# Optimization experiments

Measured on AMD Instinct MI355X. Metric: run time of the kernel, lower is better.

## Reference

```python
import jax, jax.numpy as jnp
import numpy as np

N, NS, D, HID = 8192, 512, 1024, 1024  # nodes, num_edges, f_dim, mlp hidden (max(f_dim,128))


def layernorm(x, g, b, eps=1e-5):
    m = x.mean(-1, keepdims=True)
    v = x.var(-1, keepdims=True)
    return (x - m) / jnp.sqrt(v + eps) * g + b


def mask_topk(a, kk):
    # keep only the top-kk entries of each row (vectorized version of mask_attn)
    _, idx = jax.lax.top_k(a, kk)
    rows = jnp.arange(a.shape[0])[:, None]
    mask = jnp.zeros(a.shape, a.dtype).at[rows, idx].set(1.0)
    return a * mask


def setup_inputs() -> dict:
    key = jax.random.key(0)
    ks = jax.random.split(key, 16)
    xavier = lambda k, i, o: jax.random.uniform(k, (i, o), jnp.float32, -1.0, 1.0) * np.sqrt(6.0 / (i + o))
    return {
        "inputs": jax.random.normal(ks[0], (N, D), jnp.float32),
        "noise": jax.random.normal(ks[1], (NS, D), jnp.float32),
        "edges_mu": jax.random.normal(ks[2], (1, D), jnp.float32),
        "edges_logsigma": xavier(ks[3], 1, D),
        "Wq": xavier(ks[4], D, D), "bq": jnp.zeros((D,), jnp.float32),
        "Wk": xavier(ks[5], D, D), "bk": jnp.zeros((D,), jnp.float32),
        "Wv": xavier(ks[6], D, D), "bv": jnp.zeros((D,), jnp.float32),
        "W1": xavier(ks[7], 2 * D, HID), "b1": jnp.zeros((HID,), jnp.float32),
        "W2": xavier(ks[8], HID, D), "b2": jnp.zeros((D,), jnp.float32),
        "g_in": jnp.ones((D,), jnp.float32), "b_in": jnp.zeros((D,), jnp.float32),
        "g_e": jnp.ones((D,), jnp.float32), "b_e": jnp.zeros((D,), jnp.float32),
        "k_n": 64,
        "k_e": 8,
    }


def reference(inputs, noise, edges_mu, edges_logsigma, Wq, bq, Wk, bk, Wv, bv,
              W1, b1, W2, b2, g_in, b_in, g_e, b_e, k_n, k_e):
    n, d = inputs.shape
    scale = d ** -0.5
    eps = 1e-8
    x = layernorm(inputs, g_in, b_in)                       # norm_input
    k = jax.nn.relu(x @ Wk + bk)                            # [N, D]
    v = jax.nn.relu(x @ Wv + bv)                            # [N, D]
    edges = edges_mu + jnp.exp(edges_logsigma) * noise      # [NS, D]
    # single iteration (iters=1)
    edges = layernorm(edges, g_e, b_e)                      # norm_edgs
    q = jax.nn.relu(edges @ Wq + bq)                        # [NS, D]
    dots = jnp.einsum('ni,mi->nm', q, k) * scale            # [NS, N]
    attn = jax.nn.softmax(dots, axis=1) + eps
    attn = attn / attn.sum(axis=1, keepdims=True)
    attn = mask_topk(attn, k_n)
    updates = jnp.einsum('nm,md->nd', attn, v)              # [NS, D]
    edges = jnp.concatenate([edges, updates], axis=1)       # [NS, 2D]
    edges = jax.nn.relu(edges @ W1 + b1) @ W2 + b2          # mlp -> [NS, D]
    q2 = x @ Wq + bq                                        # no relu in source
    k2 = jax.nn.relu(edges @ Wk + bk)                       # [NS, D]
    dots_v = jnp.einsum('ni,mi->nm', q2, k2) * scale        # [N, NS]
    attn_v = jax.nn.softmax(dots_v, axis=1)
    H = mask_topk(attn_v, k_e)
    return edges, H, dots
```

## Files before the change

kernel.cpp:

```cpp
#include <hip/hip_runtime.h>
#include <stdint.h>
#include <stddef.h>

typedef unsigned short u16;
typedef uint32_t u32;
typedef __bf16 bf16x8 __attribute__((ext_vector_type(8)));
typedef float f32x4 __attribute__((ext_vector_type(4)));

#define DEV __device__ __forceinline__

#define GLD16(g, l) __builtin_amdgcn_global_load_lds( \
    (const __attribute__((address_space(1))) u32*)(g), \
    (__attribute__((address_space(3))) u32*)(l), 16, 0, 0)

DEV float bf2f(u16 u){ union{uint32_t i; float f;} c; c.i=(uint32_t)u<<16; return c.f; }
DEV u16 f2bf(float f){ union{float f; uint32_t i;} c; c.f=f; uint32_t x=c.i;
  uint32_t r = x + 0x7FFFu + ((x>>16)&1u); return (u16)(r>>16); }
DEV uint32_t fmap(float f){ union{float f; uint32_t u;} c; c.f=f;
  return (c.u & 0x80000000u) ? ~c.u : (c.u | 0x80000000u); }
DEV float funmap(uint32_t u){ union{uint32_t u; float f;} c;
  c.u = (u & 0x80000000u) ? (u & 0x7FFFFFFFu) : ~u; return c.f; }
DEV void split2(float x, u16& h, u16& l){ h = f2bf(x); l = f2bf(x - bf2f(h)); }

DEV float bredsum(float v, float* buf, int tid){
  #pragma unroll
  for(int o=32;o;o>>=1) v += __shfl_down(v,o);
  __syncthreads();
  if((tid&63)==0) buf[tid>>6]=v;
  __syncthreads();
  return buf[0]+buf[1]+buf[2]+buf[3];
}
DEV float bredmax(float v, float* buf, int tid){
  #pragma unroll
  for(int o=32;o;o>>=1) v = fmaxf(v, __shfl_down(v,o));
  __syncthreads();
  if((tid&63)==0) buf[tid>>6]=v;
  __syncthreads();
  return fmaxf(fmaxf(buf[0],buf[1]),fmaxf(buf[2],buf[3]));
}
DEV int bredsumi(int v, int* buf, int tid){
  #pragma unroll
  for(int o=32;o;o>>=1) v += __shfl_down(v,o);
  __syncthreads();
  if((tid&63)==0) buf[tid>>6]=v;
  __syncthreads();
  return buf[0]+buf[1]+buf[2]+buf[3];
}

template<bool RELU, int SK>
__global__ __launch_bounds__(256)
void gemm1_64(const u16* __restrict__ A, int lda,
              const u16* __restrict__ Bt, int ldb,
              const float* __restrict__ bias, float scale,
              u16* __restrict__ outb, float* __restrict__ outf,
              float* __restrict__ part,
              int K, int ldc, int M)
{
  __shared__ __align__(16) u16 As[64*32];
  __shared__ __align__(16) u16 Bs[128*32];
  const int tid = threadIdx.x, lane = tid&63, wave = tid>>6;
  const int m0 = blockIdx.y*64, n0 = blockIdx.x*128;
  const int wm = (wave>>1)*32, wn = (wave&1)*64;
  const int ml = lane&15, quad = lane>>4;
  const int ks = K / SK;
  const int kbeg = blockIdx.z * ks;
  const u16* pa  = A  + (size_t)(m0+(tid>>2))*lda + kbeg + (tid&3)*8;
  const u16* pb0 = Bt + (size_t)(n0+(tid>>2))*ldb + kbeg + (tid&3)*8;
  const u16* pb1 = Bt + (size_t)(n0+64+(tid>>2))*ldb + kbeg + (tid&3)*8;

  f32x4 acc[2][4];
  #pragma unroll
  for(int i=0;i<2;i++)
    #pragma unroll
    for(int j=0;j<4;j++) acc[i][j] = (f32x4){0.f,0.f,0.f,0.f};

  for(int k0=0;k0<ks;k0+=32){
    __syncthreads();
    GLD16(pa +k0, &As[tid*8]);
    GLD16(pb0+k0, &Bs[tid*8]);
    GLD16(pb1+k0, &Bs[(256+tid)*8]);
    __syncthreads();
    bf16x8 af[2], bf[4];
    #pragma unroll
    for(int mi=0;mi<2;mi++) af[mi] = *(const bf16x8*)&As[(wm+mi*16+ml)*32 + quad*8];
    #pragma unroll
    for(int ni=0;ni<4;ni++) bf[ni] = *(const bf16x8*)&Bs[(wn+ni*16+ml)*32 + quad*8];
    #pragma unroll
    for(int mi=0;mi<2;mi++)
      #pragma unroll
      for(int ni=0;ni<4;ni++)
        acc[mi][ni] = __builtin_amdgcn_mfma_f32_16x16x32_bf16(af[mi], bf[ni], acc[mi][ni], 0,0,0);
  }
  #pragma unroll
  for(int mi=0;mi<2;mi++){
    const int rbase = m0 + wm + mi*16 + quad*4;
    #pragma unroll
    for(int ni=0;ni<4;ni++){
      const int col = n0 + wn + ni*16 + ml;
      if(SK==1){
        const float bv = bias ? bias[col] : 0.f;
        #pragma unroll
        for(int r=0;r<4;r++){
          float v = acc[mi][ni][r]*scale + bv;
          if(RELU) v = fmaxf(v, 0.f);
          const size_t idx = (size_t)(rbase + r)*ldc + col;
          if(outb) outb[idx] = f2bf(v);
          if(outf) outf[idx] = v;
        }
      }else{
        #pragma unroll
        for(int r=0;r<4;r++)
          part[((size_t)blockIdx.z*M + rbase + r)*ldc + col] = acc[mi][ni][r];
      }
    }
  }
}

template<bool RELU>
__global__ __launch_bounds__(256)
void gemm1_128(const u16* __restrict__ A, int lda,
               const u16* __restrict__ Bt, int ldb,
               const float* __restrict__ bias, float scale,
               u16* __restrict__ outb, float* __restrict__ outf,
               int K, int ldc)
{
  __shared__ __align__(16) u16 As[128*32];
  __shared__ __align__(16) u16 Bs[128*32];
  const int tid = threadIdx.x, lane = tid&63, wave = tid>>6;
  const int m0 = blockIdx.y*128, n0 = blockIdx.x*128;
  const int wm = (wave>>1)*64, wn = (wave&1)*64;
  const int ml = lane&15, quad = lane>>4;
  const u16* pa0 = A  + (size_t)(m0+(tid>>2))*lda    + (tid&3)*8;
  const u16* pa1 = A  + (size_t)(m0+64+(tid>>2))*lda + (tid&3)*8;
  const u16* pb0 = Bt + (size_t)(n0+(tid>>2))*ldb    + (tid&3)*8;
  const u16* pb1 = Bt + (size_t)(n0+64+(tid>>2))*ldb + (tid&3)*8;

  f32x4 acc[4][4];
  #pragma unroll
  for(int i=0;i<4;i++)
    #pragma unroll
    for(int j=0;j<4;j++) acc[i][j] = (f32x4){0.f,0.f,0.f,0.f};

  for(int k0=0;k0<K;k0+=32){
    __syncthreads();
    GLD16(pa0+k0, &As[tid*8]);
    GLD16(pa1+k0, &As[(256+tid)*8]);
    GLD16(pb0+k0, &Bs[tid*8]);
    GLD16(pb1+k0, &Bs[(256+tid)*8]);
    __syncthreads();
    bf16x8 af[4], bf[4];
    #pragma unroll
    for(int mi=0;mi<4;mi++) af[mi] = *(const bf16x8*)&As[(wm+mi*16+ml)*32 + quad*8];
    #pragma unroll
    for(int ni=0;ni<4;ni++) bf[ni] = *(const bf16x8*)&Bs[(wn+ni*16+ml)*32 + quad*8];
    #pragma unroll
    for(int mi=0;mi<4;mi++)
      #pragma unroll
      for(int ni=0;ni<4;ni++)
        acc[mi][ni] = __builtin_amdgcn_mfma_f32_16x16x32_bf16(af[mi], bf[ni], acc[mi][ni], 0,0,0);
  }
  #pragma unroll
  for(int mi=0;mi<4;mi++){
    const int rbase = m0 + wm + mi*16 + quad*4;
    #pragma unroll
    for(int ni=0;ni<4;ni++){
      const int col = n0 + wn + ni*16 + ml;
      const float bv = bias ? bias[col] : 0.f;
      #pragma unroll
      for(int r=0;r<4;r++){
        float v = acc[mi][ni][r]*scale + bv;
        if(RELU) v = fmaxf(v, 0.f);
        const size_t idx = (size_t)(rbase + r)*ldc + col;
        if(outb) outb[idx] = f2bf(v);
        if(outf) outf[idx] = v;
      }
    }
  }
}

__global__ __launch_bounds__(256)
void gemm_kv_128(const u16* __restrict__ A, int lda,
                 const u16* __restrict__ Bt, int ldb,
                 const float* __restrict__ bk, const float* __restrict__ bv,
                 u16* __restrict__ kb, u16* __restrict__ vb, int K)
{
  __shared__ __align__(16) u16 As[128*32];
  __shared__ __align__(16) u16 Bs[128*32];
  const int tid = threadIdx.x, lane = tid&63, wave = tid>>6;
  const int m0 = blockIdx.y*128, n0 = blockIdx.x*128;
  const int wm = (wave>>1)*64, wn = (wave&1)*64;
  const int ml = lane&15, quad = lane>>4;
  const u16* pa0 = A  + (size_t)(m0+(tid>>2))*lda    + (tid&3)*8;
  const u16* pa1 = A  + (size_t)(m0+64+(tid>>2))*lda + (tid&3)*8;
  const u16* pb0 = Bt + (size_t)(n0+(tid>>2))*ldb    + (tid&3)*8;
  const u16* pb1 = Bt + (size_t)(n0+64+(tid>>2))*ldb + (tid&3)*8;

  f32x4 acc[4][4];
  #pragma unroll
  for(int i=0;i<4;i++)
    #pragma unroll
    for(int j=0;j<4;j++) acc[i][j] = (f32x4){0.f,0.f,0.f,0.f};

  for(int k0=0;k0<K;k0+=32){
    __syncthreads();
    GLD16(pa0+k0, &As[tid*8]);
    GLD16(pa1+k0, &As[(256+tid)*8]);
    GLD16(pb0+k0, &Bs[tid*8]);
    GLD16(pb1+k0, &Bs[(256+tid)*8]);
    __syncthreads();
    bf16x8 af[4], bf[4];
    #pragma unroll
    for(int mi=0;mi<4;mi++) af[mi] = *(const bf16x8*)&As[(wm+mi*16+ml)*32 + quad*8];
    #pragma unroll
    for(int ni=0;ni<4;ni++) bf[ni] = *(const bf16x8*)&Bs[(wn+ni*16+ml)*32 + quad*8];
    #pragma unroll
    for(int mi=0;mi<4;mi++)
      #pragma unroll
      for(int ni=0;ni<4;ni++)
        acc[mi][ni] = __builtin_amdgcn_mfma_f32_16x16x32_bf16(af[mi], bf[ni], acc[mi][ni], 0,0,0);
  }
  #pragma unroll
  for(int mi=0;mi<4;mi++){
    const int rbase = m0 + wm + mi*16 + quad*4;
    #pragma unroll
    for(int ni=0;ni<4;ni++){
      const int col = n0 + wn + ni*16 + ml;
      const bool isv = col >= 1024;
      const int c2 = col & 1023;
      const float bb = isv ? bv[c2] : bk[c2];
      u16* outp = isv ? vb : kb;
      #pragma unroll
      for(int r=0;r<4;r++){
        const float v = fmaxf(acc[mi][ni][r] + bb, 0.f);
        outp[(size_t)(rbase + r)*1024 + c2] = f2bf(v);
      }
    }
  }
}

template<bool RELU, int SK>
__global__ __launch_bounds__(256)
void gemm3_64(const u16* __restrict__ Ah, const u16* __restrict__ Al, int lda,
              const u16* __restrict__ Bh, const u16* __restrict__ Bl, int ldb,
              const float* __restrict__ bias, float scale,
              u16* __restrict__ outh, u16* __restrict__ outl,
              float* __restrict__ outf, float* __restrict__ part,
              int K, int ldc, int M)
{
  __shared__ __align__(16) u16 AsH[64*32];
  __shared__ __align__(16) u16 AsL[64*32];
  __shared__ __align__(16) u16 BsH[128*32];
  __shared__ __align__(16) u16 BsL[128*32];
  const int tid = threadIdx.x, lane = tid&63, wave = tid>>6;
  const int m0 = blockIdx.y*64, n0 = blockIdx.x*128;
  const int wm = (wave>>1)*32, wn = (wave&1)*64;
  const int ml = lane&15, quad = lane>>4;
  const int ks = K / SK;
  const int kbeg = blockIdx.z * ks;
  const size_t ao  = (size_t)(m0+(tid>>2))*lda + kbeg + (tid&3)*8;
  const size_t bo0 = (size_t)(n0+(tid>>2))*ldb + kbeg + (tid&3)*8;
  const size_t bo1 = (size_t)(n0+64+(tid>>2))*ldb + kbeg + (tid&3)*8;

  f32x4 acc[2][4];
  #pragma unroll
  for(int i=0;i<2;i++)
    #pragma unroll
    for(int j=0;j<4;j++) acc[i][j] = (f32x4){0.f,0.f,0.f,0.f};

  for(int k0=0;k0<ks;k0+=32){
    __syncthreads();
    GLD16(Ah+ao +k0, &AsH[tid*8]);
    GLD16(Al+ao +k0, &AsL[tid*8]);
    GLD16(Bh+bo0+k0, &BsH[tid*8]);
    GLD16(Bl+bo0+k0, &BsL[tid*8]);
    GLD16(Bh+bo1+k0, &BsH[(256+tid)*8]);
    GLD16(Bl+bo1+k0, &BsL[(256+tid)*8]);
    __syncthreads();
    bf16x8 afh[2], afl[2], bfh[4], bfl[4];
    #pragma unroll
    for(int mi=0;mi<2;mi++){
      const int o = (wm+mi*16+ml)*32 + quad*8;
      afh[mi] = *(const bf16x8*)&AsH[o];
      afl[mi] = *(const bf16x8*)&AsL[o];
    }
    #pragma unroll
    for(int ni=0;ni<4;ni++){
      const int o = (wn+ni*16+ml)*32 + quad*8;
      bfh[ni] = *(const bf16x8*)&BsH[o];
      bfl[ni] = *(const bf16x8*)&BsL[o];
    }
    #pragma unroll
    for(int mi=0;mi<2;mi++)
      #pragma unroll
      for(int ni=0;ni<4;ni++){
        acc[mi][ni] = __builtin_amdgcn_mfma_f32_16x16x32_bf16(afh[mi], bfh[ni], acc[mi][ni], 0,0,0);
        acc[mi][ni] = __builtin_amdgcn_mfma_f32_16x16x32_bf16(afh[mi], bfl[ni], acc[mi][ni], 0,0,0);
        acc[mi][ni] = __builtin_amdgcn_mfma_f32_16x16x32_bf16(afl[mi], bfh[ni], acc[mi][ni], 0,0,0);
      }
  }
  #pragma unroll
  for(int mi=0;mi<2;mi++){
    const int rbase = m0 + wm + mi*16 + quad*4;
    #pragma unroll
    for(int ni=0;ni<4;ni++){
      const int col = n0 + wn + ni*16 + ml;
      if(SK==1){
        const float bv = bias ? bias[col] : 0.f;
        #pragma unroll
        for(int r=0;r<4;r++){
          float v = acc[mi][ni][r]*scale + bv;
          if(RELU) v = fmaxf(v, 0.f);
          const size_t idx = (size_t)(rbase + r)*ldc + col;
          if(outh){ u16 h, l; split2(v, h, l); outh[idx] = h; outl[idx] = l; }
          if(outf) outf[idx] = v;
        }
      }else{
        #pragma unroll
        for(int r=0;r<4;r++)
          part[((size_t)blockIdx.z*M + rbase + r)*ldc + col] = acc[mi][ni][r];
      }
    }
  }
}

__global__ __launch_bounds__(256)
void gemm3_128(const u16* __restrict__ Ah, const u16* __restrict__ Al, int lda,
               const u16* __restrict__ Bh, const u16* __restrict__ Bl, int ldb,
               const float* __restrict__ bias, float scale,
               float* __restrict__ outf, int K, int ldc)
{
  __shared__ __align__(16) u16 AsH[128*32];
  __shared__ __align__(16) u16 AsL[128*32];
  __shared__ __align__(16) u16 BsH[128*32];
  __shared__ __align__(16) u16 BsL[128*32];
  const int tid = threadIdx.x, lane = tid&63, wave = tid>>6;
  const int m0 = blockIdx.y*128, n0 = blockIdx.x*128;
  const int wm = (wave>>1)*64, wn = (wave&1)*64;
  const int ml = lane&15, quad = lane>>4;
  const size_t ao0 = (size_t)(m0+(tid>>2))*lda    + (tid&3)*8;
  const size_t ao1 = (size_t)(m0+64+(tid>>2))*lda + (tid&3)*8;
  const size_t bo0 = (size_t)(n0+(tid>>2))*ldb    + (tid&3)*8;
  const size_t bo1 = (size_t)(n0+64+(tid>>2))*ldb + (tid&3)*8;

  f32x4 acc[4][4];
  #pragma unroll
  for(int i=0;i<4;i++)
    #pragma unroll
    for(int j=0;j<4;j++) acc[i][j] = (f32x4){0.f,0.f,0.f,0.f};

  for(int k0=0;k0<K;k0+=32){
    __syncthreads();
    GLD16(Ah+ao0+k0, &AsH[tid*8]);
    GLD16(Ah+ao1+k0, &AsH[(256+tid)*8]);
    GLD16(Al+ao0+k0, &AsL[tid*8]);
    GLD16(Al+ao1+k0, &AsL[(256+tid)*8]);
    GLD16(Bh+bo0+k0, &BsH[tid*8]);
    GLD16(Bh+bo1+k0, &BsH[(256+tid)*8]);
    GLD16(Bl+bo0+k0, &BsL[tid*8]);
    GLD16(Bl+bo1+k0, &BsL[(256+tid)*8]);
    __syncthreads();
    bf16x8 afh[4], afl[4], bfh[4], bfl[4];
    #pragma unroll
    for(int mi=0;mi<4;mi++){
      const int o = (wm+mi*16+ml)*32 + quad*8;
      afh[mi] = *(const bf16x8*)&AsH[o];
      afl[mi] = *(const bf16x8*)&AsL[o];
    }
    #pragma unroll
    for(int ni=0;ni<4;ni++){
      const int o = (wn+ni*16+ml)*32 + quad*8;
      bfh[ni] = *(const bf16x8*)&BsH[o];
      bfl[ni] = *(const bf16x8*)&BsL[o];
    }
    #pragma unroll
    for(int mi=0;mi<4;mi++)
      #pragma unroll
      for(int ni=0;ni<4;ni++){
        acc[mi][ni] = __builtin_amdgcn_mfma_f32_16x16x32_bf16(afh[mi], bfh[ni], acc[mi][ni], 0,0,0);
        acc[mi][ni] = __builtin_amdgcn_mfma_f32_16x16x32_bf16(afh[mi], bfl[ni], acc[mi][ni], 0,0,0);
        acc[mi][ni] = __builtin_amdgcn_mfma_f32_16x16x32_bf16(afl[mi], bfh[ni], acc[mi][ni], 0,0,0);
      }
  }
  #pragma unroll
  for(int mi=0;mi<4;mi++){
    const int rbase = m0 + wm + mi*16 + quad*4;
    #pragma unroll
    for(int ni=0;ni<4;ni++){
      const int col = n0 + wn + ni*16 + ml;
      const float bv = bias ? bias[col] : 0.f;
      #pragma unroll
      for(int r=0;r<4;r++){
        const float v = acc[mi][ni][r]*scale + bv;
        outf[(size_t)(rbase + r)*ldc + col] = v;
      }
    }
  }
}

template<bool RELU, int SK>
__global__ __launch_bounds__(256)
void reduce_epi(const float* __restrict__ part, const float* __restrict__ bias,
                float scale, u16* __restrict__ outh, u16* __restrict__ outl,
                u16* __restrict__ outb, float* __restrict__ outf,
                size_t MN, int N,
                const float* __restrict__ bqv, float* __restrict__ bvout)
{
  __shared__ float buf[4];
  const int tid = threadIdx.x;
  const size_t i = ((size_t)blockIdx.x*256 + tid)*4;
  float4 s = *(const float4*)(part + i);
  #pragma unroll
  for(int z=1; z<SK; z++){
    const float4 t = *(const float4*)(part + (size_t)z*MN + i);
    s.x += t.x; s.y += t.y; s.z += t.z; s.w += t.w;
  }
  const int col = (int)(i % (size_t)N);
  float4 bv = bias ? *(const float4*)(bias + col) : (float4){0.f,0.f,0.f,0.f};
  float v[4] = { s.x*scale + bv.x, s.y*scale + bv.y, s.z*scale + bv.z, s.w*scale + bv.w };
  if(RELU){
    #pragma unroll
    for(int j=0;j<4;j++) v[j] = fmaxf(v[j], 0.f);
  }
  if(outh){
    ushort4 h4, l4;
    split2(v[0], h4.x, l4.x); split2(v[1], h4.y, l4.y);
    split2(v[2], h4.z, l4.z); split2(v[3], h4.w, l4.w);
    *(ushort4*)(outh + i) = h4;
    *(ushort4*)(outl + i) = l4;
  }
  if(outb){
    ushort4 b4;
    b4.x=f2bf(v[0]); b4.y=f2bf(v[1]); b4.z=f2bf(v[2]); b4.w=f2bf(v[3]);
    *(ushort4*)(outb + i) = b4;
  }
  if(outf) *(float4*)(outf + i) = (float4){v[0],v[1],v[2],v[3]};
  if(bvout){
    const float4 q = *(const float4*)(bqv + col);
    float d = q.x*v[0] + q.y*v[1] + q.z*v[2] + q.w*v[3];
    d = bredsum(d, buf, tid);
    if(tid==0) bvout[blockIdx.x] = d * 0.03125f;
  }
}

DEV void dev_tsplit(const float* in, u16* oh, u16* ol, int R, int C,
                    int bx, int by, int tid, float (*tile)[33])
{
  const int tx = tid & 31, ty = tid >> 5;
  #pragma unroll
  for(int i=0;i<32;i+=8)
    tile[ty+i][tx] = in[(size_t)(by*32+ty+i)*C + bx*32 + tx];
  __syncthreads();
  #pragma unroll
  for(int i=0;i<32;i+=8){
    const float v = tile[tx][ty+i];
    u16 h, l; split2(v, h, l);
    const size_t o = (size_t)(bx*32+ty+i)*R + by*32 + tx;
    oh[o] = h; if(ol) ol[o] = l;
  }
}
__global__ __launch_bounds__(256)
void prep_weights(const float* __restrict__ Wk, const float* __restrict__ W1,
                  const float* __restrict__ W2, const float* __restrict__ Wv,
                  const float* __restrict__ Wq,
                  u16* __restrict__ WkvTh, u16* __restrict__ WkTl,
                  u16* __restrict__ W1Th,  u16* __restrict__ W1Tl,
                  u16* __restrict__ W2Th,  u16* __restrict__ W2Tl,
                  u16* __restrict__ WqTh,
                  u16* __restrict__ Wqh,   u16* __restrict__ Wql)
{
  __shared__ float tile[32][33];
  const int id = blockIdx.x, tid = threadIdx.x;
  if(id < 1024){
    dev_tsplit(Wk, WkvTh, WkTl, 1024, 1024, id&31, id>>5, tid, tile);
  }else if(id < 3072){
    const int l = id - 1024;
    dev_tsplit(W1, W1Th, W1Tl, 2048, 1024, l&31, l>>5, tid, tile);
  }else if(id < 4096){
    const int l = id - 3072;
    dev_tsplit(W2, W2Th, W2Tl, 1024, 1024, l&31, l>>5, tid, tile);
  }else if(id < 5120){
    const int l = id - 4096;
    dev_tsplit(Wv, WkvTh + 1024*1024, nullptr, 1024, 1024, l&31, l>>5, tid, tile);
  }else if(id < 6144){
    const int l = id - 5120;
    dev_tsplit(Wq, WqTh, nullptr, 1024, 1024, l&31, l>>5, tid, tile);
  }else{
    const int l = id - 6144;
    const int i = l*256 + tid;
    const float4 v = ((const float4*)Wq)[i];
    ushort4 h4, l4;
    split2(v.x, h4.x, l4.x); split2(v.y, h4.y, l4.y);
    split2(v.z, h4.z, l4.z); split2(v.w, h4.w, l4.w);
    ((ushort4*)Wqh)[i] = h4; ((ushort4*)Wql)[i] = l4;
  }
}

__global__ __launch_bounds__(256)
void ln_all(const float* __restrict__ in, const float* __restrict__ g,
            const float* __restrict__ bb, u16* __restrict__ outh,
            u16* __restrict__ outl,
            const float* __restrict__ noise, const float* __restrict__ mu,
            const float* __restrict__ lsig, const float* __restrict__ ge,
            const float* __restrict__ be, u16* __restrict__ cath,
            u16* __restrict__ catl)
{
  __shared__ float buf[4];
  const int tid = threadIdx.x;
  const bool edge = blockIdx.x >= 8192;
  const int row = edge ? (blockIdx.x - 8192) : blockIdx.x;
  float v0,v1,v2,v3;
  if(!edge){
    const float4 xv = ((const float4*)(in + (size_t)row*1024))[tid];
    v0=xv.x; v1=xv.y; v2=xv.z; v3=xv.w;
  }else{
    const float4 nv  = ((const float4*)(noise + (size_t)row*1024))[tid];
    const float4 muv = ((const float4*)mu)[tid];
    const float4 lsv = ((const float4*)lsig)[tid];
    v0 = muv.x + expf(lsv.x)*nv.x;
    v1 = muv.y + expf(lsv.y)*nv.y;
    v2 = muv.z + expf(lsv.z)*nv.z;
    v3 = muv.w + expf(lsv.w)*nv.w;
  }
  float s  = bredsum(v0+v1+v2+v3, buf, tid);
  float s2 = bredsum(v0*v0+v1*v1+v2*v2+v3*v3, buf, tid);
  const float mean = s * (1.f/1024.f);
  const float var  = s2 * (1.f/1024.f) - mean*mean;
  const float rs   = 1.f / sqrtf(var + 1e-5f);
  const float4 gv = ((const float4*)(edge?ge:g))[tid];
  const float4 bv = ((const float4*)(edge?be:bb))[tid];
  float o0 = (v0-mean)*rs*gv.x + bv.x;
  float o1 = (v1-mean)*rs*gv.y + bv.y;
  float o2 = (v2-mean)*rs*gv.z + bv.z;
  float o3 = (v3-mean)*rs*gv.w + bv.w;
  ushort4 oh, ol;
  split2(o0, oh.x, ol.x); split2(o1, oh.y, ol.y);
  split2(o2, oh.z, ol.z); split2(o3, oh.w, ol.w);
  u16* ph = edge ? cath : outh;
  u16* pl = edge ? catl : outl;
  const int ostride = edge ? 2048 : 1024;
  ((ushort4*)(ph + (size_t)row*ostride))[tid] = oh;
  ((ushort4*)(pl + (size_t)row*ostride))[tid] = ol;
}

#define SWZ(i) ((i) ^ (((((unsigned)(i))>>5)&7u)<<2))
__global__ __launch_bounds__(256)
void softmax_topk_a(const float* __restrict__ dots, const int* __restrict__ knp,
                    int* __restrict__ tidx, float* __restrict__ tw)
{
  const int NC = 8192;
  __shared__ __align__(16) uint32_t us[8192];
  __shared__ float fbuf[4];
  __shared__ int ibuf[4];
  __shared__ int scan[256];
  __shared__ uint32_t hist[256];
  __shared__ uint32_t bcast;
  __shared__ int slot_ctr;
  const int row = blockIdx.x, tid = threadIdx.x;
  const int lane = tid & 63, wave = tid >> 6;
  const float* x = dots + (size_t)row * NC;

  float mx = -3.4e38f;
  #pragma unroll
  for(int it=0; it<8; ++it){
    const int i = (tid + it*256)*4;
    const float4 f = *(const float4*)(x + i);
    mx = fmaxf(fmaxf(mx, fmaxf(f.x,f.y)), fmaxf(f.z,f.w));
    uint4 u; u.x=fmap(f.x); u.y=fmap(f.y); u.z=fmap(f.z); u.w=fmap(f.w);
    *(uint4*)&us[SWZ(i)] = u;
  }
  mx = bredmax(mx, fbuf, tid);

  float se = 0.f;
  #pragma unroll
  for(int it=0; it<8; ++it){
    const int i = (tid + it*256)*4;
    const uint4 u = *(const uint4*)&us[SWZ(i)];
    se += expf(funmap(u.x)-mx) + expf(funmap(u.y)-mx)
        + expf(funmap(u.z)-mx) + expf(funmap(u.w)-mx);
  }
  se = bredsum(se, fbuf, tid);
  const float T = 1.f + (float)NC * 1e-8f;

  const int k = knp[0];
  const int base = tid*32;

  uint32_t prefix = 0;
  int remaining = k;
  #pragma unroll
  for(int shift=24; shift>=0; shift-=8){
    hist[tid] = 0;
    __syncthreads();
    const uint32_t himask = (shift==24) ? 0u : (0xFFFFFFFFu << (shift+8));
    #pragma unroll
    for(int j=0;j<32;j+=4){
      const uint4 u4 = *(const uint4*)&us[SWZ(base+j)];
      const uint32_t uu[4] = {u4.x,u4.y,u4.z,u4.w};
      #pragma unroll
      for(int t=0;t<4;t++)
        if((uu[t] & himask) == prefix) atomicAdd(&hist[(uu[t]>>shift)&255u], 1u);
    }
    __syncthreads();
    if(wave==0){
      const uint32_t h0=hist[4*lane], h1=hist[4*lane+1],
                     h2=hist[4*lane+2], h3=hist[4*lane+3];
      const uint32_t s3=h3, s2=h2+s3, s1=h1+s2, s0=h0+s1;
      uint32_t tsum = s0;
      #pragma unroll
      for(int o=1;o<64;o<<=1){
        const uint32_t vv = __shfl_down(tsum, o);
        if(lane + o < 64) tsum += vv;
      }
      const uint32_t excl = tsum - s0;
      const uint32_t r = (uint32_t)remaining;
      int cand = -1; uint32_t gsel = 0;
      if     (s3+excl >= r){ cand = 4*lane+3; gsel = excl; }
      else if(s2+excl >= r){ cand = 4*lane+2; gsel = s3+excl; }
      else if(s1+excl >= r){ cand = 4*lane+1; gsel = s2+excl; }
      else if(s0+excl >= r){ cand = 4*lane+0; gsel = s1+excl; }
      int bestc = cand; uint32_t bestg = gsel;
      #pragma unroll
      for(int o=32;o;o>>=1){
        const int oc = __shfl_xor(bestc, o);
        const uint32_t og = __shfl_xor(bestg, o);
        if(oc > bestc){ bestc = oc; bestg = og; }
      }
      if(lane==0) bcast = (uint32_t)bestc;
      remaining -= (int)bestg;
    }
    __syncthreads();
    prefix |= bcast << shift;
  }
  const uint32_t uth = prefix;

  int gt = 0, eq = 0;
  #pragma unroll
  for(int j=0;j<32;j+=4){
    const uint4 u4 = *(const uint4*)&us[SWZ(base+j)];
    gt += (u4.x>uth)+(u4.y>uth)+(u4.z>uth)+(u4.w>uth);
    eq += (u4.x==uth)+(u4.y==uth)+(u4.z==uth)+(u4.w==uth);
  }
  const int c1 = bredsumi(gt, ibuf, tid);
  __syncthreads();
  scan[tid] = eq;
  __syncthreads();
  #pragma unroll
  for(int o=1;o<256;o<<=1){
    int t = (tid>=o) ? scan[tid-o] : 0;
    __syncthreads();
    scan[tid] += t;
    __syncthreads();
  }
  int eq_rank = scan[tid] - eq;
  const int budget = k - c1;
  if(tid==0) slot_ctr = 0;
  __syncthreads();
  #pragma unroll 2
  for(int j=0;j<32;j+=4){
    const uint4 u4 = *(const uint4*)&us[SWZ(base+j)];
    const uint32_t uu[4] = {u4.x,u4.y,u4.z,u4.w};
    #pragma unroll
    for(int t=0;t<4;t++){
      const uint32_t u = uu[t];
      bool sel = (u > uth);
      if(u == uth){ sel = (eq_rank < budget); eq_rank++; }
      if(sel){
        const int s = atomicAdd(&slot_ctr, 1);
        const float f = funmap(u);
        const float w = (expf(f - mx)/se + 1e-8f) / T;
        if(s < 128){ tidx[row*128 + s] = base + j + t; tw[row*128 + s] = w; }
      }
    }
  }
}

__global__ __launch_bounds__(256)
void gather_updates(const int* __restrict__ tidx, const float* __restrict__ tw,
                    const int* __restrict__ knp, const u16* __restrict__ v,
                    u16* __restrict__ cath, u16* __restrict__ catl)
{
  __shared__ int   idx_s[128];
  __shared__ float w_s[128];
  const int row = blockIdx.x, tid = threadIdx.x;
  const int kk = knp[0];
  if(tid < 128){
    idx_s[tid] = (tid < kk) ? (tidx[row*128+tid] & 8191) : 0;
    w_s[tid]   = (tid < kk) ? tw[row*128+tid] : 0.f;
  }
  __syncthreads();
  const int c = tid*4;
  float a0=0,a1=0,a2=0,a3=0;
  for(int j=0;j<kk && j<128;j++){
    const ushort4 vv = *(const ushort4*)&v[(size_t)idx_s[j]*1024 + c];
    const float w = w_s[j];
    a0 += w*bf2f(vv.x); a1 += w*bf2f(vv.y); a2 += w*bf2f(vv.z); a3 += w*bf2f(vv.w);
  }
  ushort4 oh, ol;
  split2(a0, oh.x, ol.x); split2(a1, oh.y, ol.y);
  split2(a2, oh.z, ol.z); split2(a3, oh.w, ol.w);
  ((ushort4*)(cath + (size_t)row*2048 + 1024))[tid] = oh;
  ((ushort4*)(catl + (size_t)row*2048 + 1024))[tid] = ol;
}

__global__ __launch_bounds__(256)
void softmax_topk_h_wave(const float* __restrict__ dv, const int* __restrict__ kep,
                         float* __restrict__ H)
{
  const int wave = threadIdx.x >> 6, lane = threadIdx.x & 63;
  const int row = blockIdx.x*4 + wave;
  const float* x = dv + (size_t)row*512 + lane*8;
  const float4 a = *(const float4*)x;
  const float4 b = *(const float4*)(x+4);
  float vals[8] = {a.x,a.y,a.z,a.w,b.x,b.y,b.z,b.w};

  float mx = vals[0];
  #pragma unroll
  for(int j=1;j<8;j++) mx = fmaxf(mx, vals[j]);
  #pragma unroll
  for(int o=32;o;o>>=1) mx = fmaxf(mx, __shfl_xor(mx, o));
  float e[8], se = 0.f;
  #pragma unroll
  for(int j=0;j<8;j++){ e[j] = expf(vals[j]-mx); se += e[j]; }
  #pragma unroll
  for(int o=32;o;o>>=1) se += __shfl_xor(se, o);
  const float inv = 1.f/se;

  const int k = kep[0];
  unsigned int selmask = 0;
  for(int r=0;r<k;r++){
    unsigned long long best = 0;
    #pragma unroll
    for(int j=0;j<8;j++){
      if(!((selmask>>j)&1u)){
        const unsigned long long key =
          ((unsigned long long)fmap(vals[j]) << 9) | (unsigned long long)(511 - (lane*8+j));
        if(key > best) best = key;
      }
    }
    #pragma unroll
    for(int o=32;o;o>>=1){
      const unsigned long long other = __shfl_xor(best, o);
      if(other > best) best = other;
    }
    const int bidx = 511 - (int)(best & 511ull);
    if((bidx>>3) == lane) selmask |= 1u << (bidx & 7);
  }

  float4 o0, o1;
  o0.x = (selmask&  1u) ? e[0]*inv : 0.f;
  o0.y = (selmask&  2u) ? e[1]*inv : 0.f;
  o0.z = (selmask&  4u) ? e[2]*inv : 0.f;
  o0.w = (selmask&  8u) ? e[3]*inv : 0.f;
  o1.x = (selmask& 16u) ? e[4]*inv : 0.f;
  o1.y = (selmask& 32u) ? e[5]*inv : 0.f;
  o1.z = (selmask& 64u) ? e[6]*inv : 0.f;
  o1.w = (selmask&128u) ? e[7]*inv : 0.f;
  float* outp = H + (size_t)row*512 + lane*8;
  *(float4*)outp     = o0;
  *(float4*)(outp+4) = o1;
}

extern "C" void kernel_launch(void* const* d_in, const int* in_sizes, int n_in,
                              void* d_out, int out_size, void* d_ws, size_t ws_size,
                              hipStream_t stream)
{
  const float* inputs = (const float*)d_in[0];
  const float* noise  = (const float*)d_in[1];
  const float* emu    = (const float*)d_in[2];
  const float* elsig  = (const float*)d_in[3];
  const float* Wq = (const float*)d_in[4];  const float* bq = (const float*)d_in[5];
  const float* Wk = (const float*)d_in[6];  const float* bk = (const float*)d_in[7];
  const float* Wv = (const float*)d_in[8];  const float* bv = (const float*)d_in[9];
  const float* W1 = (const float*)d_in[10]; const float* b1 = (const float*)d_in[11];
  const float* W2 = (const float*)d_in[12]; const float* b2 = (const float*)d_in[13];
  const float* g_in = (const float*)d_in[14]; const float* b_in = (const float*)d_in[15];
  const float* g_e  = (const float*)d_in[16]; const float* b_e  = (const float*)d_in[17];
  const int* knp = (const int*)d_in[18];
  const int* kep = (const int*)d_in[19];

  float* out = (float*)d_out;
  float* out_edges = out;
  float* out_H     = out + 512*1024;
  float* out_dots  = out + 512*1024 + 8192*512;

  char* p = (char*)d_ws;
  const size_t MB = 1024ull*1024;
  u16* xh = (u16*)(p + 0*MB);
  u16* xl = (u16*)(p + 16*MB);
  u16* kb = (u16*)(p + 32*MB);
  u16* vb = (u16*)(p + 48*MB);
  float* dotsvf = (float*)(p + 32*MB);
  u16* WkvTh = (u16*)(p + 64*MB);
  u16* WkTl  = (u16*)(p + 68*MB);
  u16* WqTh  = (u16*)(p + 70*MB);
  u16* Wqh   = (u16*)(p + 72*MB);  u16* Wql  = (u16*)(p + 74*MB);
  u16* W1Th  = (u16*)(p + 76*MB);  u16* W1Tl = (u16*)(p + 80*MB);
  u16* W2Th  = (u16*)(p + 84*MB);  u16* W2Tl = (u16*)(p + 86*MB);
  u16* cath = (u16*)(p + 88*MB);  u16* catl = (u16*)(p + 90*MB);
  u16* qmb  = (u16*)(p + 92*MB);
  u16* h1h  = (u16*)(p + 93*MB);  u16* h1l  = (u16*)(p + 94*MB);
  u16* eoh  = (u16*)(p + 95*MB);  u16* eol  = (u16*)(p + 96*MB);
  u16* k2h  = (u16*)(p + 97*MB);  u16* k2l  = (u16*)(p + 98*MB);
  u16* Gth  = (u16*)(p + 99*MB);  u16* Gtl  = (u16*)(p + 100*MB);
  int*   tidx  = (int*)  (p + 101*MB);
  float* tw    = (float*)(p + 101*MB + 256*1024);
  float* biasv = (float*)(p + 101*MB + 512*1024);
  float* part  = (float*)(p + 104*MB);

  hipMemsetAsync(tidx, 0, 512ull*128*4*2, stream);

  prep_weights<<<7168,256,0,stream>>>(Wk, W1, W2, Wv, Wq,
                                      WkvTh, WkTl, W1Th, W1Tl, W2Th, W2Tl,
                                      WqTh, Wqh, Wql);
  ln_all<<<8704,256,0,stream>>>(inputs, g_in, b_in, xh, xl,
                                noise, emu, elsig, g_e, b_e, cath, catl);

  const size_t MN = 512ull*1024;
  gemm_kv_128<<<dim3(16,64),256,0,stream>>>(xh,1024, WkvTh,1024, bk, bv,
                                            kb, vb, 1024);
  gemm1_64<false,4><<<dim3(8,8,4),256,0,stream>>>(cath,2048, WqTh,1024, nullptr, 1.f,
                                                  nullptr,nullptr, part, 1024,1024,512);
  reduce_epi<true,4><<<512,256,0,stream>>>(part, bq, 1.f, nullptr,nullptr, qmb,nullptr,
                                           MN, 1024, nullptr, nullptr);
  gemm1_128<false><<<dim3(64,4),256,0,stream>>>(qmb,1024, kb,1024, nullptr, 0.03125f,
                                                nullptr,out_dots, 1024,8192);
  softmax_topk_a<<<512,256,0,stream>>>(out_dots, knp, tidx, tw);
  gather_updates<<<512,256,0,stream>>>(tidx, tw, knp, vb, cath, catl);

  gemm3_64<false,4><<<dim3(8,8,4),256,0,stream>>>(cath,catl,2048, W1Th,W1Tl,2048,
                                                  nullptr,1.f, nullptr,nullptr,nullptr,
                                                  part, 2048,1024,512);
  reduce_epi<true,4><<<512,256,0,stream>>>(part, b1, 1.f, h1h,h1l, nullptr,nullptr,
                                           MN, 1024, nullptr, nullptr);
  gemm3_64<false,4><<<dim3(8,8,4),256,0,stream>>>(h1h,h1l,1024, W2Th,W2Tl,1024,
                                                  nullptr,1.f, nullptr,nullptr,nullptr,
                                                  part, 1024,1024,512);
  reduce_epi<false,4><<<512,256,0,stream>>>(part, b2, 1.f, eoh,eol, nullptr,out_edges,
                                            MN, 1024, nullptr, nullptr);
  gemm3_64<false,4><<<dim3(8,8,4),256,0,stream>>>(eoh,eol,1024, WkvTh,WkTl,1024,
                                                  nullptr,1.f, nullptr,nullptr,nullptr,
                                                  part, 1024,1024,512);
  reduce_epi<true,4><<<512,256,0,stream>>>(part, bk, 1.f, k2h,k2l, nullptr,nullptr,
                                           MN, 1024, bq, biasv);
  gemm3_64<false,4><<<dim3(8,8,4),256,0,stream>>>(k2h,k2l,1024, Wqh,Wql,1024,
                                                  nullptr,1.f, nullptr,nullptr,nullptr,
                                                  part, 1024,1024,512);
  reduce_epi<false,4><<<512,256,0,stream>>>(part, nullptr, 1.f, Gth,Gtl, nullptr,nullptr,
                                            MN, 1024, nullptr, nullptr);
  gemm3_128<<<dim3(4,64),256,0,stream>>>(xh,xl,1024, Gth,Gtl,1024,
                                         biasv, 0.03125f, dotsvf, 1024,512);
  softmax_topk_h_wave<<<2048,256,0,stream>>>(dotsvf, kep, out_H);
}
```

Measured before the change: 426.8 us.

## Double-buffer LDS tiles in GEMM kernels to overlap loads with MFMA

Converts the five GEMM kernels from single-buffered LDS staging with two barriers per K-step to a double-buffered scheme. The next K-slice is prefetched into the alternate buffer via global_load_lds while MFMAs consume the current one, leaving one barrier per iteration. This is meant to hide global-load latency behind compute. In exchange LDS use per block doubles, up to 64KB for gemm3_128, which may lower occupancy. Correctness depends on the single barrier also draining the async LDS loads before the buffer is read.

```diff
diff --git a/kernel.cpp b/kernel.cpp
--- a/kernel.cpp
+++ b/kernel.cpp
@@ -56,8 +56,8 @@
               float* __restrict__ part,
               int K, int ldc, int M)
 {
-  __shared__ __align__(16) u16 As[64*32];
-  __shared__ __align__(16) u16 Bs[128*32];
+  __shared__ __align__(16) u16 As[2][64*32];
+  __shared__ __align__(16) u16 Bs[2][128*32];
   const int tid = threadIdx.x, lane = tid&63, wave = tid>>6;
   const int m0 = blockIdx.y*64, n0 = blockIdx.x*128;
   const int wm = (wave>>1)*32, wn = (wave&1)*64;
@@ -74,22 +74,30 @@
     #pragma unroll
     for(int j=0;j<4;j++) acc[i][j] = (f32x4){0.f,0.f,0.f,0.f};
 
+  GLD16(pa , &As[0][tid*8]);
+  GLD16(pb0, &Bs[0][tid*8]);
+  GLD16(pb1, &Bs[0][(256+tid)*8]);
+  __syncthreads();
+  int cur = 0;
   for(int k0=0;k0<ks;k0+=32){
-    __syncthreads();
-    GLD16(pa +k0, &As[tid*8]);
-    GLD16(pb0+k0, &Bs[tid*8]);
-    GLD16(pb1+k0, &Bs[(256+tid)*8]);
-    __syncthreads();
+    const int nxt = cur^1;
+    if(k0+32<ks){
+      GLD16(pa +k0+32, &As[nxt][tid*8]);
+      GLD16(pb0+k0+32, &Bs[nxt][tid*8]);
+      GLD16(pb1+k0+32, &Bs[nxt][(256+tid)*8]);
+    }
     bf16x8 af[2], bf[4];
     #pragma unroll
-    for(int mi=0;mi<2;mi++) af[mi] = *(const bf16x8*)&As[(wm+mi*16+ml)*32 + quad*8];
-    #pragma unroll
-    for(int ni=0;ni<4;ni++) bf[ni] = *(const bf16x8*)&Bs[(wn+ni*16+ml)*32 + quad*8];
+    for(int mi=0;mi<2;mi++) af[mi] = *(const bf16x8*)&As[cur][(wm+mi*16+ml)*32 + quad*8];
+    #pragma unroll
+    for(int ni=0;ni<4;ni++) bf[ni] = *(const bf16x8*)&Bs[cur][(wn+ni*16+ml)*32 + quad*8];
     #pragma unroll
     for(int mi=0;mi<2;mi++)
       #pragma unroll
       for(int ni=0;ni<4;ni++)
         acc[mi][ni] = __builtin_amdgcn_mfma_f32_16x16x32_bf16(af[mi], bf[ni], acc[mi][ni], 0,0,0);
+    __syncthreads();
+    cur = nxt;
   }
   #pragma unroll
   for(int mi=0;mi<2;mi++){
@@ -124,8 +132,8 @@
                u16* __restrict__ outb, float* __restrict__ outf,
                int K, int ldc)
 {
-  __shared__ __align__(16) u16 As[128*32];
-  __shared__ __align__(16) u16 Bs[128*32];
+  __shared__ __align__(16) u16 As[2][128*32];
+  __shared__ __align__(16) u16 Bs[2][128*32];
   const int tid = threadIdx.x, lane = tid&63, wave = tid>>6;
   const int m0 = blockIdx.y*128, n0 = blockIdx.x*128;
   const int wm = (wave>>1)*64, wn = (wave&1)*64;
@@ -141,23 +149,32 @@
     #pragma unroll
     for(int j=0;j<4;j++) acc[i][j] = (f32x4){0.f,0.f,0.f,0.f};
 
+  GLD16(pa0, &As[0][tid*8]);
+  GLD16(pa1, &As[0][(256+tid)*8]);
+  GLD16(pb0, &Bs[0][tid*8]);
+  GLD16(pb1, &Bs[0][(256+tid)*8]);
+  __syncthreads();
+  int cur = 0;
   for(int k0=0;k0<K;k0+=32){
-    __syncthreads();
-    GLD16(pa0+k0, &As[tid*8]);
-    GLD16(pa1+k0, &As[(256+tid)*8]);
-    GLD16(pb0+k0, &Bs[tid*8]);
-    GLD16(pb1+k0, &Bs[(256+tid)*8]);
-    __syncthreads();
+    const int nxt = cur^1;
+    if(k0+32<K){
+      GLD16(pa0+k0+32, &As[nxt][tid*8]);
+      GLD16(pa1+k0+32, &As[nxt][(256+tid)*8]);
+      GLD16(pb0+k0+32, &Bs[nxt][tid*8]);
+      GLD16(pb1+k0+32, &Bs[nxt][(256+tid)*8]);
+    }
     bf16x8 af[4], bf[4];
     #pragma unroll
-    for(int mi=0;mi<4;mi++) af[mi] = *(const bf16x8*)&As[(wm+mi*16+ml)*32 + quad*8];
-    #pragma unroll
-    for(int ni=0;ni<4;ni++) bf[ni] = *(const bf16x8*)&Bs[(wn+ni*16+ml)*32 + quad*8];
+    for(int mi=0;mi<4;mi++) af[mi] = *(const bf16x8*)&As[cur][(wm+mi*16+ml)*32 + quad*8];
+    #pragma unroll
+    for(int ni=0;ni<4;ni++) bf[ni] = *(const bf16x8*)&Bs[cur][(wn+ni*16+ml)*32 + quad*8];
     #pragma unroll
     for(int mi=0;mi<4;mi++)
       #pragma unroll
       for(int ni=0;ni<4;ni++)
         acc[mi][ni] = __builtin_amdgcn_mfma_f32_16x16x32_bf16(af[mi], bf[ni], acc[mi][ni], 0,0,0);
+    __syncthreads();
+    cur = nxt;
   }
   #pragma unroll
   for(int mi=0;mi<4;mi++){
@@ -184,8 +201,8 @@
                  const float* __restrict__ bk, const float* __restrict__ bv,
                  u16* __restrict__ kb, u16* __restrict__ vb, int K)
 {
-  __shared__ __align__(16) u16 As[128*32];
-  __shared__ __align__(16) u16 Bs[128*32];
+  __shared__ __align__(16) u16 As[2][128*32];
+  __shared__ __align__(16) u16 Bs[2][128*32];
   const int tid = threadIdx.x, lane = tid&63, wave = tid>>6;
   const int m0 = blockIdx.y*128, n0 = blockIdx.x*128;
   const int wm = (wave>>1)*64, wn = (wave&1)*64;
@@ -201,23 +218,32 @@
     #pragma unroll
     for(int j=0;j<4;j++) acc[i][j] = (f32x4){0.f,0.f,0.f,0.f};
 
+  GLD16(pa0, &As[0][tid*8]);
+  GLD16(pa1, &As[0][(256+tid)*8]);
+  GLD16(pb0, &Bs[0][tid*8]);
+  GLD16(pb1, &Bs[0][(256+tid)*8]);
+  __syncthreads();
+  int cur = 0;
   for(int k0=0;k0<K;k0+=32){
-    __syncthreads();
-    GLD16(pa0+k0, &As[tid*8]);
-    GLD16(pa1+k0, &As[(256+tid)*8]);
-    GLD16(pb0+k0, &Bs[tid*8]);
-    GLD16(pb1+k0, &Bs[(256+tid)*8]);
-    __syncthreads();
+    const int nxt = cur^1;
+    if(k0+32<K){
+      GLD16(pa0+k0+32, &As[nxt][tid*8]);
+      GLD16(pa1+k0+32, &As[nxt][(256+tid)*8]);
+      GLD16(pb0+k0+32, &Bs[nxt][tid*8]);
+      GLD16(pb1+k0+32, &Bs[nxt][(256+tid)*8]);
+    }
     bf16x8 af[4], bf[4];
     #pragma unroll
-    for(int mi=0;mi<4;mi++) af[mi] = *(const bf16x8*)&As[(wm+mi*16+ml)*32 + quad*8];
-    #pragma unroll
-    for(int ni=0;ni<4;ni++) bf[ni] = *(const bf16x8*)&Bs[(wn+ni*16+ml)*32 + quad*8];
+    for(int mi=0;mi<4;mi++) af[mi] = *(const bf16x8*)&As[cur][(wm+mi*16+ml)*32 + quad*8];
+    #pragma unroll
+    for(int ni=0;ni<4;ni++) bf[ni] = *(const bf16x8*)&Bs[cur][(wn+ni*16+ml)*32 + quad*8];
     #pragma unroll
     for(int mi=0;mi<4;mi++)
       #pragma unroll
       for(int ni=0;ni<4;ni++)
         acc[mi][ni] = __builtin_amdgcn_mfma_f32_16x16x32_bf16(af[mi], bf[ni], acc[mi][ni], 0,0,0);
+    __syncthreads();
+    cur = nxt;
   }
   #pragma unroll
   for(int mi=0;mi<4;mi++){
@@ -247,19 +273,22 @@
               float* __restrict__ outf, float* __restrict__ part,
               int K, int ldc, int M)
 {
-  __shared__ __align__(16) u16 AsH[64*32];
-  __shared__ __align__(16) u16 AsL[64*32];
-  __shared__ __align__(16) u16 BsH[128*32];
-  __shared__ __align__(16) u16 BsL[128*32];
+  __shared__ __align__(16) u16 AsH[2][64*32];
+  __shared__ __align__(16) u16 AsL[2][64*32];
+  __shared__ __align__(16) u16 BsH[2][128*32];
+  __shared__ __align__(16) u16 BsL[2][128*32];
   const int tid = threadIdx.x, lane = tid&63, wave = tid>>6;
   const int m0 = blockIdx.y*64, n0 = blockIdx.x*128;
   const int wm = (wave>>1)*32, wn = (wave&1)*64;
   const int ml = lane&15, quad = lane>>4;
   const int ks = K / SK;
   const int kbeg = blockIdx.z * ks;
-  const size_t ao  = (size_t)(m0+(tid>>2))*lda + kbeg + (tid&3)*8;
-  const size_t bo0 = (size_t)(n0+(tid>>2))*ldb + kbeg + (tid&3)*8;
-  const size_t bo1 = (size_t)(n0+64+(tid>>2))*ldb + kbeg + (tid&3)*8;
+  const u16* pah  = Ah + (size_t)(m0+(tid>>2))*lda + kbeg + (tid&3)*8;
+  const u16* pal  = Al + (size_t)(m0+(tid>>2))*lda + kbeg + (tid&3)*8;
+  const u16* pbh0 = Bh + (size_t)(n0+(tid>>2))*ldb + kbeg + (tid&3)*8;
+  const u16* pbl0 = Bl + (size_t)(n0+(tid>>2))*ldb + kbeg + (tid&3)*8;
+  const u16* pbh1 = Bh + (size_t)(n0+64+(tid>>2))*ldb + kbeg + (tid&3)*8;
+  const u16* pbl1 = Bl + (size_t)(n0+64+(tid>>2))*ldb + kbeg + (tid&3)*8;
 
   f32x4 acc[2][4];
   #pragma unroll
@@ -267,27 +296,36 @@
     #pragma unroll
     for(int j=0;j<4;j++) acc[i][j] = (f32x4){0.f,0.f,0.f,0.f};
 
+  GLD16(pah , &AsH[0][tid*8]);
+  GLD16(pal , &AsL[0][tid*8]);
+  GLD16(pbh0, &BsH[0][tid*8]);
+  GLD16(pbl0, &BsL[0][tid*8]);
+  GLD16(pbh1, &BsH[0][(256+tid)*8]);
+  GLD16(pbl1, &BsL[0][(256+tid)*8]);
+  __syncthreads();
+  int cur = 0;
   for(int k0=0;k0<ks;k0+=32){
-    __syncthreads();
-    GLD16(Ah+ao +k0, &AsH[tid*8]);
-    GLD16(Al+ao +k0, &AsL[tid*8]);
-    GLD16(Bh+bo0+k0, &BsH[tid*8]);
-    GLD16(Bl+bo0+k0, &BsL[tid*8]);
-    GLD16(Bh+bo1+k0, &BsH[(256+tid)*8]);
-    GLD16(Bl+bo1+k0, &BsL[(256+tid)*8]);
-    __syncthreads();
+    const int nxt = cur^1;
+    if(k0+32<ks){
+      GLD16(pah +k0+32, &AsH[nxt][tid*8]);
+      GLD16(pal +k0+32, &AsL[nxt][tid*8]);
+      GLD16(pbh0+k0+32, &BsH[nxt][tid*8]);
+      GLD16(pbl0+k0+32, &BsL[nxt][tid*8]);
+      GLD16(pbh1+k0+32, &BsH[nxt][(256+tid)*8]);
+      GLD16(pbl1+k0+32, &BsL[nxt][(256+tid)*8]);
+    }
     bf16x8 afh[2], afl[2], bfh[4], bfl[4];
     #pragma unroll
     for(int mi=0;mi<2;mi++){
       const int o = (wm+mi*16+ml)*32 + quad*8;
-      afh[mi] = *(const bf16x8*)&AsH[o];
-      afl[mi] = *(const bf16x8*)&AsL[o];
+      afh[mi] = *(const bf16x8*)&AsH[cur][o];
+      afl[mi] = *(const bf16x8*)&AsL[cur][o];
     }
     #pragma unroll
     for(int ni=0;ni<4;ni++){
       const int o = (wn+ni*16+ml)*32 + quad*8;
-      bfh[ni] = *(const bf16x8*)&BsH[o];
-      bfl[ni] = *(const bf16x8*)&BsL[o];
+      bfh[ni] = *(const bf16x8*)&BsH[cur][o];
+      bfl[ni] = *(const bf16x8*)&BsL[cur][o];
     }
     #pragma unroll
     for(int mi=0;mi<2;mi++)
@@ -297,6 +335,8 @@
         acc[mi][ni] = __builtin_amdgcn_mfma_f32_16x16x32_bf16(afh[mi], bfl[ni], acc[mi][ni], 0,0,0);
         acc[mi][ni] = __builtin_amdgcn_mfma_f32_16x16x32_bf16(afl[mi], bfh[ni], acc[mi][ni], 0,0,0);
       }
+    __syncthreads();
+    cur = nxt;
   }
   #pragma unroll
   for(int mi=0;mi<2;mi++){
@@ -329,18 +369,22 @@
                const float* __restrict__ bias, float scale,
                float* __restrict__ outf, int K, int ldc)
 {
-  __shared__ __align__(16) u16 AsH[128*32];
-  __shared__ __align__(16) u16 AsL[128*32];
-  __shared__ __align__(16) u16 BsH[128*32];
-  __shared__ __align__(16) u16 BsL[128*32];
+  __shared__ __align__(16) u16 AsH[2][128*32];
+  __shared__ __align__(16) u16 AsL[2][128*32];
+  __shared__ __align__(16) u16 BsH[2][128*32];
+  __shared__ __align__(16) u16 BsL[2][128*32];
   const int tid = threadIdx.x, lane = tid&63, wave = tid>>6;
   const int m0 = blockIdx.y*128, n0 = blockIdx.x*128;
   const int wm = (wave>>1)*64, wn = (wave&1)*64;
   const int ml = lane&15, quad = lane>>4;
-  const size_t ao0 = (size_t)(m0+(tid>>2))*lda    + (tid&3)*8;
-  const size_t ao1 = (size_t)(m0+64+(tid>>2))*lda + (tid&3)*8;
-  const size_t bo0 = (size_t)(n0+(tid>>2))*ldb    + (tid&3)*8;
-  const size_t bo1 = (size_t)(n0+64+(tid>>2))*ldb + (tid&3)*8;
+  const u16* pah0 = Ah + (size_t)(m0+(tid>>2))*lda    + (tid&3)*8;
+  const u16* pah1 = Ah + (size_t)(m0+64+(tid>>2))*lda + (tid&3)*8;
+  const u16* pal0 = Al + (size_t)(m0+(tid>>2))*lda    + (tid&3)*8;
+  const u16* pal1 = Al + (size_t)(m0+64+(tid>>2))*lda + (tid&3)*8;
+  const u16* pbh0 = Bh + (size_t)(n0+(tid>>2))*ldb    + (tid&3)*8;
+  const u16* pbh1 = Bh + (size_t)(n0+64+(tid>>2))*ldb + (tid&3)*8;
+  const u16* pbl0 = Bl + (size_t)(n0+(tid>>2))*ldb    + (tid&3)*8;
+  const u16* pbl1 = Bl + (size_t)(n0+64+(tid>>2))*ldb + (tid&3)*8;
 
   f32x4 acc[4][4];
   #pragma unroll
@@ -348,29 +392,40 @@
     #pragma unroll
     for(int j=0;j<4;j++) acc[i][j] = (f32x4){0.f,0.f,0.f,0.f};
 
+  GLD16(pah0, &AsH[0][tid*8]);
+  GLD16(pah1, &AsH[0][(256+tid)*8]);
+  GLD16(pal0, &AsL[0][tid*8]);
+  GLD16(pal1, &AsL[0][(256+tid)*8]);
+  GLD16(pbh0, &BsH[0][tid*8]);
+  GLD16(pbh1, &BsH[0][(256+tid)*8]);
+  GLD16(pbl0, &BsL[0][tid*8]);
+  GLD16(pbl1, &BsL[0][(256+tid)*8]);
+  __syncthreads();
+  int cur = 0;
   for(int k0=0;k0<K;k0+=32){
-    __syncthreads();
-    GLD16(Ah+ao0+k0, &AsH[tid*8]);
-    GLD16(Ah+ao1+k0, &AsH[(256+tid)*8]);
-    GLD16(Al+ao0+k0, &AsL[tid*8]);
-    GLD16(Al+ao1+k0, &AsL[(256+tid)*8]);
-    GLD16(Bh+bo0+k0, &BsH[tid*8]);
-    GLD16(Bh+bo1+k0, &BsH[(256+tid)*8]);
-    GLD16(Bl+bo0+k0, &BsL[tid*8]);
-    GLD16(Bl+bo1+k0, &BsL[(256+tid)*8]);
-    __syncthreads();
+    const int nxt = cur^1;
+    if(k0+32<K){
+      GLD16(pah0+k0+32, &AsH[nxt][tid*8]);
+      GLD16(pah1+k0+32, &AsH[nxt][(256+tid)*8]);
+      GLD16(pal0+k0+32, &AsL[nxt][tid*8]);
+      GLD16(pal1+k0+32, &AsL[nxt][(256+tid)*8]);
+      GLD16(pbh0+k0+32, &BsH[nxt][tid*8]);
+      GLD16(pbh1+k0+32, &BsH[nxt][(256+tid)*8]);
+      GLD16(pbl0+k0+32, &BsL[nxt][tid*8]);
+      GLD16(pbl1+k0+32, &BsL[nxt][(256+tid)*8]);
+    }
     bf16x8 afh[4], afl[4], bfh[4], bfl[4];
     #pragma unroll
     for(int mi=0;mi<4;mi++){
       const int o = (wm+mi*16+ml)*32 + quad*8;
-      afh[mi] = *(const bf16x8*)&AsH[o];
-      afl[mi] = *(const bf16x8*)&AsL[o];
+      afh[mi] = *(const bf16x8*)&AsH[cur][o];
+      afl[mi] = *(const bf16x8*)&AsL[cur][o];
     }
     #pragma unroll
     for(int ni=0;ni<4;ni++){
       const int o = (wn+ni*16+ml)*32 + quad*8;
-      bfh[ni] = *(const bf16x8*)&BsH[o];
-      bfl[ni] = *(const bf16x8*)&BsL[o];
+      bfh[ni] = *(const bf16x8*)&BsH[cur][o];
+      bfl[ni] = *(const bf16x8*)&BsL[cur][o];
     }
     #pragma unroll
     for(int mi=0;mi<4;mi++)
@@ -380,6 +435,8 @@
         acc[mi][ni] = __builtin_amdgcn_mfma_f32_16x16x32_bf16(afh[mi], bfl[ni], acc[mi][ni], 0,0,0);
         acc[mi][ni] = __builtin_amdgcn_mfma_f32_16x16x32_bf16(afl[mi], bfh[ni], acc[mi][ni], 0,0,0);
       }
+    __syncthreads();
+    cur = nxt;
   }
   #pragma unroll
   for(int mi=0;mi<4;mi++){
```

After: 417.9 us. -2.1%, faster.
